# Performance work log

Measured on AMD Instinct MI355X. Metric: run time of the kernel, lower is better.

The kernel has to match this reference:

```python
import jax, jax.numpy as jnp
import numpy as np

D_MODEL = 1024
NUM_HEADS = 16
DEPTH = D_MODEL // NUM_HEADS


def setup_inputs() -> dict:
    key = jax.random.key(0)
    ks = jax.random.split(key, 12)
    B, S = 4, 2048
    scale = 1.0 / np.sqrt(D_MODEL)
    inp = {
        "query": jax.random.normal(ks[0], (B, S, D_MODEL), dtype=jnp.float32),
        "key": jax.random.normal(ks[1], (B, S, D_MODEL), dtype=jnp.float32),
        "value": jax.random.normal(ks[2], (B, S, D_MODEL), dtype=jnp.float32),
        "mask": jnp.zeros((B, 1, 1, S), dtype=jnp.float32),  # 1.0 = masked position
        "Wq": jax.random.normal(ks[3], (D_MODEL, D_MODEL), dtype=jnp.float32) * scale,
        "bq": jnp.zeros((D_MODEL,), dtype=jnp.float32),
        "Wk": jax.random.normal(ks[4], (D_MODEL, D_MODEL), dtype=jnp.float32) * scale,
        "bk": jnp.zeros((D_MODEL,), dtype=jnp.float32),
        "Wv": jax.random.normal(ks[5], (D_MODEL, D_MODEL), dtype=jnp.float32) * scale,
        "bv": jnp.zeros((D_MODEL,), dtype=jnp.float32),
        "Wo": jax.random.normal(ks[6], (D_MODEL, D_MODEL), dtype=jnp.float32) * scale,
        "bo": jnp.zeros((D_MODEL,), dtype=jnp.float32),
    }
    return inp


def _split_heads(x):
    # [B, S, D] -> [B, H, S, depth]
    B, S, _ = x.shape
    return x.reshape(B, S, NUM_HEADS, DEPTH).transpose(0, 2, 1, 3)


def reference(query, key, value, mask, Wq, bq, Wk, bk, Wv, bv, Wo, bo):
    B, Sq, _ = query.shape
    q = _split_heads(query @ Wq + bq)   # [B, H, Sq, d]
    k = _split_heads(key @ Wk + bk)     # [B, H, Sk, d]
    v = _split_heads(value @ Wv + bv)   # [B, H, Sk, d]
    logits = jnp.einsum('bhqd,bhkd->bhqk', q, k) / jnp.sqrt(jnp.float32(DEPTH))
    logits = logits + mask * (-1e9)
    attn = jax.nn.softmax(logits, axis=-1)
    ctx = jnp.einsum('bhqk,bhkd->bhqd', attn, v)        # [B, H, Sq, d]
    ctx = ctx.transpose(0, 2, 1, 3).reshape(B, Sq, D_MODEL)
    return ctx @ Wo + bo
```

## Files before the change

kernel.cpp:

```cpp
#include <hip/hip_runtime.h>
#include <math.h>

#define BB 4
#define SS 2048
#define DDM 1024
#define HH 16
#define MM (BB * SS)

typedef _Float16 f16;
typedef f16 half8 __attribute__((ext_vector_type(8)));
typedef f16 f16x4 __attribute__((ext_vector_type(4)));
typedef float f32x4 __attribute__((ext_vector_type(4)));

#define GLOAD16(g, l)                                                  \
  __builtin_amdgcn_global_load_lds(                                    \
      (const __attribute__((address_space(1))) void*)(g),              \
      (__attribute__((address_space(3))) void*)(l), 16, 0, 0)

__global__ void cvt_f16_k(const float* __restrict__ in, f16* __restrict__ out,
                          int n4) {
  int i = blockIdx.x * blockDim.x + threadIdx.x;
  const int stride = gridDim.x * blockDim.x;
  for (; i < n4; i += stride) {
    const float4 v = reinterpret_cast<const float4*>(in)[i];
    f16x4 o;
    o.x = (f16)v.x; o.y = (f16)v.y; o.z = (f16)v.z; o.w = (f16)v.w;
    reinterpret_cast<f16x4*>(out)[i] = o;
  }
}

__global__ void wtr_k(const float* __restrict__ W, f16* __restrict__ Wt) {
  __shared__ float t[32][33];
  const int bx = blockIdx.x * 32, by = blockIdx.y * 32;
  const int tx = threadIdx.x, ty = threadIdx.y;
#pragma unroll
  for (int i = 0; i < 4; ++i)
    t[ty + i * 8][tx] = W[(size_t)(by + ty + i * 8) * DDM + bx + tx];
  __syncthreads();
#pragma unroll
  for (int i = 0; i < 4; ++i)
    Wt[(size_t)(bx + ty + i * 8) * DDM + by + tx] = (f16)t[tx][ty + i * 8];
}

__global__ __launch_bounds__(256, 2) void gemm_f16_k(
    const f16* __restrict__ A, const f16* __restrict__ Bt,
    const float* __restrict__ bias, void* __restrict__ out, int mode) {
  __shared__ f16 Al[2][128 * 64];
  __shared__ f16 Bl[2][128 * 64];
  const int tid = threadIdx.x;
  const int l = tid & 63, w = tid >> 6;
  const int lr = l & 15, lg = l >> 4;
  const int wr = w >> 1, wc = w & 1;
  const int bm = blockIdx.x << 7, bn = blockIdx.y << 7;

  f32x4 acc[4][4];
#pragma unroll
  for (int m = 0; m < 4; ++m)
#pragma unroll
    for (int n = 0; n < 4; ++n) acc[m][n] = (f32x4){0.f, 0.f, 0.f, 0.f};

  const int srow = tid >> 3;
  const int scol = (tid & 7) ^ (srow & 7);
  const f16* Ap = A + (size_t)(bm + srow) * DDM + scol * 8;
  const f16* Bp = Bt + (size_t)(bn + srow) * DDM + scol * 8;
  const int kx = lr & 7;

#define G_STAGE(buf, kk)                                                     \
  do {                                                                       \
    _Pragma("unroll") for (int it = 0; it < 4; ++it) {                       \
      GLOAD16(Ap + (size_t)(it * 32) * DDM + (kk),                           \
              &Al[buf][(it * 256 + w * 64) * 8]);                            \
      GLOAD16(Bp + (size_t)(it * 32) * DDM + (kk),                           \
              &Bl[buf][(it * 256 + w * 64) * 8]);                            \
    }                                                                        \
  } while (0)

  G_STAGE(0, 0);
  __syncthreads();

  for (int kk = 0; kk < DDM; kk += 64) {
    const int cur = (kk >> 6) & 1;
    if (kk + 64 < DDM) G_STAGE(cur ^ 1, kk + 64);
#pragma unroll
    for (int kh = 0; kh < 2; ++kh) {
      half8 af[4], bf[4];
#pragma unroll
      for (int m = 0; m < 4; ++m) {
        const int row = wr * 64 + m * 16 + lr;
        af[m] = *reinterpret_cast<const half8*>(
            &Al[cur][row * 64 + (((kh * 4 + lg) ^ kx) * 8)]);
      }
#pragma unroll
      for (int n = 0; n < 4; ++n) {
        const int row = wc * 64 + n * 16 + lr;
        bf[n] = *reinterpret_cast<const half8*>(
            &Bl[cur][row * 64 + (((kh * 4 + lg) ^ kx) * 8)]);
      }
#pragma unroll
      for (int m = 0; m < 4; ++m)
#pragma unroll
        for (int n = 0; n < 4; ++n)
          acc[m][n] = __builtin_amdgcn_mfma_f32_16x16x32_f16(af[m], bf[n],
                                                             acc[m][n], 0, 0, 0);
    }
    __syncthreads();
  }
#undef G_STAGE

#pragma unroll
  for (int n = 0; n < 4; ++n) {
    const int gn = bn + wc * 64 + n * 16 + lr;
    const float bv = bias[gn];
#pragma unroll
    for (int m = 0; m < 4; ++m) {
      const int gm0 = bm + wr * 64 + m * 16 + lg * 4;
      if (mode == 2) {
        const int b = gm0 >> 11, s = gm0 & (SS - 1);
        const int h = gn >> 6, d = gn & 63;
        f16x4 o;
#pragma unroll
        for (int r = 0; r < 4; ++r) o[r] = (f16)(acc[m][n][r] + bv);
        *reinterpret_cast<f16x4*>(
            reinterpret_cast<f16*>(out) +
            (((size_t)(b * HH + h) * 64 + d) * SS + s)) = o;
      } else {
#pragma unroll
        for (int r = 0; r < 4; ++r) {
          const int gm = gm0 + r;
          const float v = acc[m][n][r] + bv;
          if (mode == 0) {
            reinterpret_cast<float*>(out)[(size_t)gm * DDM + gn] = v;
          } else {
            const int b = gm >> 11, s = gm & (SS - 1);
            const int h = gn >> 6, d = gn & 63;
            reinterpret_cast<f16*>(
                out)[(((size_t)(b * HH + h) * SS + s) << 6) + d] = (f16)v;
          }
        }
      }
    }
  }
}

__global__ __launch_bounds__(256, 2) void attn_f16_k(
    const f16* __restrict__ Q, const f16* __restrict__ K,
    const f16* __restrict__ Vt, const float* __restrict__ mask,
    f16* __restrict__ ctx) {
  __shared__ f16 Kl[2][64 * 64];
  __shared__ f16 Vl[2][64 * 64];
  __shared__ f16 Pl[4 * 16 * 66];
  __shared__ float Ml[SS];

  const int tid = threadIdx.x;
  const int l = tid & 63, w = tid >> 6;
  const int lr = l & 15, lg = l >> 4;
  const int qt = blockIdx.x;
  const int bh = blockIdx.y;
  const int b = bh >> 4, h = bh & 15;

  for (int i = tid; i < SS; i += 256) Ml[i] = mask[(size_t)b * SS + i] * -1e9f;

  const size_t qrow = (size_t)bh * SS + qt * 64 + w * 16 + lr;
  half8 qf0 = *reinterpret_cast<const half8*>(Q + qrow * 64 + lg * 8);
  half8 qf1 = *reinterpret_cast<const half8*>(Q + qrow * 64 + 32 + lg * 8);

  float m_s[4], l_s[4];
  f32x4 oa[4];
#pragma unroll
  for (int r = 0; r < 4; ++r) { m_s[r] = -1e30f; l_s[r] = 0.f; }
#pragma unroll
  for (int n = 0; n < 4; ++n) oa[n] = (f32x4){0.f, 0.f, 0.f, 0.f};

  const f16* Kg = K + (size_t)bh * SS * 64;
  const f16* Vg = Vt + (size_t)bh * 64 * SS;

  const int srow = tid >> 3;
  const int scol = (tid & 7) ^ (srow & 7);
  const int kx = lr & 7;
  f16* Pw = Pl + w * (16 * 66);

#define A_STAGE(buf, kt)                                                     \
  do {                                                                       \
    const f16* Kt_ = Kg + (size_t)(kt) * 64 * 64;                            \
    GLOAD16(Kt_ + srow * 64 + scol * 8, &Kl[buf][(w * 64) * 8]);             \
    GLOAD16(Kt_ + (32 + srow) * 64 + scol * 8,                               \
            &Kl[buf][(256 + w * 64) * 8]);                                   \
    const f16* Vr_ = Vg + (size_t)(kt) * 64 + scol * 8;                      \
    GLOAD16(Vr_ + (size_t)srow * SS, &Vl[buf][(w * 64) * 8]);                \
    GLOAD16(Vr_ + (size_t)(32 + srow) * SS, &Vl[buf][(256 + w * 64) * 8]);   \
  } while (0)

  A_STAGE(0, 0);
  __syncthreads();

  for (int kt = 0; kt < 32; ++kt) {
    const int cur = kt & 1;
    if (kt + 1 < 32) A_STAGE(cur ^ 1, kt + 1);

    f32x4 sv[4];
#pragma unroll
    for (int n = 0; n < 4; ++n) {
      f32x4 s = (f32x4){0.f, 0.f, 0.f, 0.f};
      const int krow = (n * 16 + lr) * 64;
      half8 kf0 = *reinterpret_cast<const half8*>(
          &Kl[cur][krow + ((lg ^ kx) * 8)]);
      half8 kf1 = *reinterpret_cast<const half8*>(
          &Kl[cur][krow + (((4 + lg) ^ kx) * 8)]);
      s = __builtin_amdgcn_mfma_f32_16x16x32_f16(qf0, kf0, s, 0, 0, 0);
      s = __builtin_amdgcn_mfma_f32_16x16x32_f16(qf1, kf1, s, 0, 0, 0);
      const float mk = Ml[kt * 64 + n * 16 + lr];
#pragma unroll
      for (int r = 0; r < 4; ++r) sv[n][r] = s[r] * 0.125f + mk;
    }

#pragma unroll
    for (int r = 0; r < 4; ++r) {
      float mx = fmaxf(fmaxf(sv[0][r], sv[1][r]), fmaxf(sv[2][r], sv[3][r]));
      mx = fmaxf(mx, __shfl_xor(mx, 1));
      mx = fmaxf(mx, __shfl_xor(mx, 2));
      mx = fmaxf(mx, __shfl_xor(mx, 4));
      mx = fmaxf(mx, __shfl_xor(mx, 8));
      const float mn = fmaxf(m_s[r], mx);
      const float corr = __expf(m_s[r] - mn);
      float sum = 0.f;
#pragma unroll
      for (int n = 0; n < 4; ++n) {
        const float p = __expf(sv[n][r] - mn);
        sv[n][r] = p;
        sum += p;
      }
      sum += __shfl_xor(sum, 1);
      sum += __shfl_xor(sum, 2);
      sum += __shfl_xor(sum, 4);
      sum += __shfl_xor(sum, 8);
      l_s[r] = l_s[r] * corr + sum;
      m_s[r] = mn;
#pragma unroll
      for (int n = 0; n < 4; ++n) oa[n][r] *= corr;
    }

#pragma unroll
    for (int n = 0; n < 4; ++n)
#pragma unroll
      for (int r = 0; r < 4; ++r)
        Pw[(lg * 4 + r) * 66 + n * 16 + lr] = (f16)sv[n][r];

    half8 pa0 = *reinterpret_cast<const half8*>(Pw + lr * 66 + lg * 8);
    half8 pa1 = *reinterpret_cast<const half8*>(Pw + lr * 66 + 32 + lg * 8);
#pragma unroll
    for (int n = 0; n < 4; ++n) {
      const int vrow = (n * 16 + lr) * 64;
      half8 vf0 = *reinterpret_cast<const half8*>(
          &Vl[cur][vrow + ((lg ^ kx) * 8)]);
      half8 vf1 = *reinterpret_cast<const half8*>(
          &Vl[cur][vrow + (((4 + lg) ^ kx) * 8)]);
      oa[n] = __builtin_amdgcn_mfma_f32_16x16x32_f16(pa0, vf0, oa[n], 0, 0, 0);
      oa[n] = __builtin_amdgcn_mfma_f32_16x16x32_f16(pa1, vf1, oa[n], 0, 0, 0);
    }
    __syncthreads();
  }
#undef A_STAGE

#pragma unroll
  for (int r = 0; r < 4; ++r) {
    const float inv = 1.0f / l_s[r];
    const int s_g = qt * 64 + w * 16 + lg * 4 + r;
#pragma unroll
    for (int n = 0; n < 4; ++n)
      ctx[((size_t)b * SS + s_g) * DDM + h * 64 + n * 16 + lr] =
          (f16)(oa[n][r] * inv);
  }
}

extern "C" void kernel_launch(void* const* d_in, const int* in_sizes, int n_in,
                              void* d_out, int out_size, void* d_ws,
                              size_t ws_size, hipStream_t stream) {
  const float* query = (const float*)d_in[0];
  const float* key   = (const float*)d_in[1];
  const float* value = (const float*)d_in[2];
  const float* mask  = (const float*)d_in[3];
  const float* Wq = (const float*)d_in[4];
  const float* bq = (const float*)d_in[5];
  const float* Wk = (const float*)d_in[6];
  const float* bk = (const float*)d_in[7];
  const float* Wv = (const float*)d_in[8];
  const float* bv = (const float*)d_in[9];
  const float* Wo = (const float*)d_in[10];
  const float* bo = (const float*)d_in[11];
  float* out = (float*)d_out;

  const size_t E = (size_t)MM * DDM;
  f16* ws = (f16*)d_ws;
  f16* Qh = ws;
  f16* Kh = Qh + E;
  f16* Vh = Kh + E;
  f16* Wt0 = Vh + E;
  f16* Wt1 = Wt0 + (size_t)DDM * DDM;
  f16* Wt2 = Wt1 + (size_t)DDM * DDM;
  f16* Wt3 = Wt2 + (size_t)DDM * DDM;
  f16* Qp = Wt3 + (size_t)DDM * DDM;
  f16* Kp = Qp + E;
  f16* Vp = Kp + E;
  f16* Ch = Vp + E;

  const int n4 = (int)(E / 4);
  cvt_f16_k<<<2048, 256, 0, stream>>>(query, Qh, n4);
  cvt_f16_k<<<2048, 256, 0, stream>>>(key, Kh, n4);
  cvt_f16_k<<<2048, 256, 0, stream>>>(value, Vh, n4);
  dim3 tb(32, 8), tg(32, 32);
  wtr_k<<<tg, tb, 0, stream>>>(Wq, Wt0);
  wtr_k<<<tg, tb, 0, stream>>>(Wk, Wt1);
  wtr_k<<<tg, tb, 0, stream>>>(Wv, Wt2);
  wtr_k<<<tg, tb, 0, stream>>>(Wo, Wt3);

  dim3 gg(MM / 128, DDM / 128);
  gemm_f16_k<<<gg, 256, 0, stream>>>(Qh, Wt0, bq, Qp, 1);
  gemm_f16_k<<<gg, 256, 0, stream>>>(Kh, Wt1, bk, Kp, 1);
  gemm_f16_k<<<gg, 256, 0, stream>>>(Vh, Wt2, bv, Vp, 2);
  attn_f16_k<<<dim3(SS / 64, BB * HH), 256, 0, stream>>>(Qp, Kp, Vp, mask, Ch);
  gemm_f16_k<<<gg, 256, 0, stream>>>(Ch, Wt3, bo, out, 0);
}
```

Before: 525.8 us.

## Double attention query tile, lazy rescale, single-buffer GEMM, merge prep kernels

The attention kernel now handles 128 query rows per block (32 per wave), so each K/V tile loaded into LDS is reused across twice as many rows. It pre-scales Q by 1/8, uses exp2 with log2e folded in, and rescales the running output only when a row max increases. The mask is read directly from global memory instead of being staged in LDS. The GEMM drops LDS double buffering to raise occupancy (launch bounds 4), at the cost of exposing load latency behind a barrier every k-step, and the convert and transpose launches are merged into single kernels.

```diff
diff --git a/kernel.cpp b/kernel.cpp
--- a/kernel.cpp
+++ b/kernel.cpp
@@ -17,20 +17,28 @@
       (const __attribute__((address_space(1))) void*)(g),              \
       (__attribute__((address_space(3))) void*)(l), 16, 0, 0)
 
-__global__ void cvt_f16_k(const float* __restrict__ in, f16* __restrict__ out,
-                          int n4) {
+__global__ void cvt3_k(const float* __restrict__ q, const float* __restrict__ k,
+                       const float* __restrict__ v, f16* __restrict__ oq,
+                       f16* __restrict__ ok, f16* __restrict__ ov, int n4) {
+  const float* in = (blockIdx.y == 0) ? q : (blockIdx.y == 1) ? k : v;
+  f16* out = (blockIdx.y == 0) ? oq : (blockIdx.y == 1) ? ok : ov;
   int i = blockIdx.x * blockDim.x + threadIdx.x;
   const int stride = gridDim.x * blockDim.x;
   for (; i < n4; i += stride) {
-    const float4 v = reinterpret_cast<const float4*>(in)[i];
+    const float4 t = reinterpret_cast<const float4*>(in)[i];
     f16x4 o;
-    o.x = (f16)v.x; o.y = (f16)v.y; o.z = (f16)v.z; o.w = (f16)v.w;
+    o.x = (f16)t.x; o.y = (f16)t.y; o.z = (f16)t.z; o.w = (f16)t.w;
     reinterpret_cast<f16x4*>(out)[i] = o;
   }
 }
 
-__global__ void wtr_k(const float* __restrict__ W, f16* __restrict__ Wt) {
+__global__ void wtr4_k(const float* __restrict__ Wq, const float* __restrict__ Wk,
+                       const float* __restrict__ Wv, const float* __restrict__ Wo,
+                       f16* __restrict__ Wt_all) {
   __shared__ float t[32][33];
+  const int z = blockIdx.z;
+  const float* W = (z == 0) ? Wq : (z == 1) ? Wk : (z == 2) ? Wv : Wo;
+  f16* Wt = Wt_all + (size_t)z * DDM * DDM;
   const int bx = blockIdx.x * 32, by = blockIdx.y * 32;
   const int tx = threadIdx.x, ty = threadIdx.y;
 #pragma unroll
@@ -42,11 +50,11 @@
     Wt[(size_t)(bx + ty + i * 8) * DDM + by + tx] = (f16)t[tx][ty + i * 8];
 }
 
-__global__ __launch_bounds__(256, 2) void gemm_f16_k(
+__global__ __launch_bounds__(256, 4) void gemm_f16_k(
     const f16* __restrict__ A, const f16* __restrict__ Bt,
     const float* __restrict__ bias, void* __restrict__ out, int mode) {
-  __shared__ f16 Al[2][128 * 64];
-  __shared__ f16 Bl[2][128 * 64];
+  __shared__ f16 Al[128 * 64];
+  __shared__ f16 Bl[128 * 64];
   const int tid = threadIdx.x;
   const int l = tid & 63, w = tid >> 6;
   const int lr = l & 15, lg = l >> 4;
@@ -65,22 +73,13 @@
   const f16* Bp = Bt + (size_t)(bn + srow) * DDM + scol * 8;
   const int kx = lr & 7;
 
-#define G_STAGE(buf, kk)                                                     \
-  do {                                                                       \
-    _Pragma("unroll") for (int it = 0; it < 4; ++it) {                       \
-      GLOAD16(Ap + (size_t)(it * 32) * DDM + (kk),                           \
-              &Al[buf][(it * 256 + w * 64) * 8]);                            \
-      GLOAD16(Bp + (size_t)(it * 32) * DDM + (kk),                           \
-              &Bl[buf][(it * 256 + w * 64) * 8]);                            \
-    }                                                                        \
-  } while (0)
-
-  G_STAGE(0, 0);
-  __syncthreads();
-
   for (int kk = 0; kk < DDM; kk += 64) {
-    const int cur = (kk >> 6) & 1;
-    if (kk + 64 < DDM) G_STAGE(cur ^ 1, kk + 64);
+#pragma unroll
+    for (int it = 0; it < 4; ++it) {
+      GLOAD16(Ap + (size_t)(it * 32) * DDM + kk, Al + (it * 256 + w * 64) * 8);
+      GLOAD16(Bp + (size_t)(it * 32) * DDM + kk, Bl + (it * 256 + w * 64) * 8);
+    }
+    __syncthreads();
 #pragma unroll
     for (int kh = 0; kh < 2; ++kh) {
       half8 af[4], bf[4];
@@ -88,13 +87,13 @@
       for (int m = 0; m < 4; ++m) {
         const int row = wr * 64 + m * 16 + lr;
         af[m] = *reinterpret_cast<const half8*>(
-            &Al[cur][row * 64 + (((kh * 4 + lg) ^ kx) * 8)]);
+            Al + row * 64 + (((kh * 4 + lg) ^ kx) * 8));
       }
 #pragma unroll
       for (int n = 0; n < 4; ++n) {
         const int row = wc * 64 + n * 16 + lr;
         bf[n] = *reinterpret_cast<const half8*>(
-            &Bl[cur][row * 64 + (((kh * 4 + lg) ^ kx) * 8)]);
+            Bl + row * 64 + (((kh * 4 + lg) ^ kx) * 8));
       }
 #pragma unroll
       for (int m = 0; m < 4; ++m)
@@ -105,7 +104,6 @@
     }
     __syncthreads();
   }
-#undef G_STAGE
 
 #pragma unroll
   for (int n = 0; n < 4; ++n) {
@@ -142,14 +140,13 @@
   }
 }
 
-__global__ __launch_bounds__(256, 2) void attn_f16_k(
+__global__ __launch_bounds__(256, 3) void attn_f16_k(
     const f16* __restrict__ Q, const f16* __restrict__ K,
     const f16* __restrict__ Vt, const float* __restrict__ mask,
     f16* __restrict__ ctx) {
   __shared__ f16 Kl[2][64 * 64];
   __shared__ f16 Vl[2][64 * 64];
-  __shared__ f16 Pl[4 * 16 * 66];
-  __shared__ float Ml[SS];
+  __shared__ f16 Pl[4][32 * 66];
 
   const int tid = threadIdx.x;
   const int l = tid & 63, w = tid >> 6;
@@ -158,26 +155,42 @@
   const int bh = blockIdx.y;
   const int b = bh >> 4, h = bh & 15;
 
-  for (int i = tid; i < SS; i += 256) Ml[i] = mask[(size_t)b * SS + i] * -1e9f;
-
-  const size_t qrow = (size_t)bh * SS + qt * 64 + w * 16 + lr;
-  half8 qf0 = *reinterpret_cast<const half8*>(Q + qrow * 64 + lg * 8);
-  half8 qf1 = *reinterpret_cast<const half8*>(Q + qrow * 64 + 32 + lg * 8);
-
-  float m_s[4], l_s[4];
-  f32x4 oa[4];
-#pragma unroll
-  for (int r = 0; r < 4; ++r) { m_s[r] = -1e30f; l_s[r] = 0.f; }
-#pragma unroll
-  for (int n = 0; n < 4; ++n) oa[n] = (f32x4){0.f, 0.f, 0.f, 0.f};
+  const float LOG2E = 1.44269504f;
+  const float NEGML2 = -1e9f * 1.44269504f;
+
+  half8 qf[2][2];
+  const size_t qbase = (size_t)bh * SS + qt * 128 + w * 32;
+#pragma unroll
+  for (int m = 0; m < 2; ++m) {
+    const size_t qrow = qbase + m * 16 + lr;
+#pragma unroll
+    for (int hh = 0; hh < 2; ++hh) {
+      half8 v = *reinterpret_cast<const half8*>(Q + qrow * 64 + hh * 32 + lg * 8);
+#pragma unroll
+      for (int j = 0; j < 8; ++j) v[j] = v[j] * (f16)0.125f;
+      qf[m][hh] = v;
+    }
+  }
+
+  float m_s[2][4], l_s[2][4];
+  f32x4 oa[2][4];
+#pragma unroll
+  for (int m = 0; m < 2; ++m)
+#pragma unroll
+    for (int r = 0; r < 4; ++r) { m_s[m][r] = -1e30f; l_s[m][r] = 0.f; }
+#pragma unroll
+  for (int m = 0; m < 2; ++m)
+#pragma unroll
+    for (int n = 0; n < 4; ++n) oa[m][n] = (f32x4){0.f, 0.f, 0.f, 0.f};
 
   const f16* Kg = K + (size_t)bh * SS * 64;
   const f16* Vg = Vt + (size_t)bh * 64 * SS;
+  const float* mrow = mask + (size_t)b * SS;
 
   const int srow = tid >> 3;
   const int scol = (tid & 7) ^ (srow & 7);
   const int kx = lr & 7;
-  f16* Pw = Pl + w * (16 * 66);
+  f16* Pw = Pl[w];
 
 #define A_STAGE(buf, kt)                                                     \
   do {                                                                       \
@@ -197,56 +210,82 @@
     const int cur = kt & 1;
     if (kt + 1 < 32) A_STAGE(cur ^ 1, kt + 1);
 
-    f32x4 sv[4];
+    float mk[4];
+#pragma unroll
+    for (int n = 0; n < 4; ++n) mk[n] = mrow[kt * 64 + n * 16 + lr] * NEGML2;
+
+    f32x4 sv[2][4];
 #pragma unroll
     for (int n = 0; n < 4; ++n) {
-      f32x4 s = (f32x4){0.f, 0.f, 0.f, 0.f};
       const int krow = (n * 16 + lr) * 64;
       half8 kf0 = *reinterpret_cast<const half8*>(
           &Kl[cur][krow + ((lg ^ kx) * 8)]);
       half8 kf1 = *reinterpret_cast<const half8*>(
           &Kl[cur][krow + (((4 + lg) ^ kx) * 8)]);
-      s = __builtin_amdgcn_mfma_f32_16x16x32_f16(qf0, kf0, s, 0, 0, 0);
-      s = __builtin_amdgcn_mfma_f32_16x16x32_f16(qf1, kf1, s, 0, 0, 0);
-      const float mk = Ml[kt * 64 + n * 16 + lr];
-#pragma unroll
-      for (int r = 0; r < 4; ++r) sv[n][r] = s[r] * 0.125f + mk;
-    }
-
-#pragma unroll
-    for (int r = 0; r < 4; ++r) {
-      float mx = fmaxf(fmaxf(sv[0][r], sv[1][r]), fmaxf(sv[2][r], sv[3][r]));
-      mx = fmaxf(mx, __shfl_xor(mx, 1));
-      mx = fmaxf(mx, __shfl_xor(mx, 2));
-      mx = fmaxf(mx, __shfl_xor(mx, 4));
-      mx = fmaxf(mx, __shfl_xor(mx, 8));
-      const float mn = fmaxf(m_s[r], mx);
-      const float corr = __expf(m_s[r] - mn);
-      float sum = 0.f;
-#pragma unroll
-      for (int n = 0; n < 4; ++n) {
-        const float p = __expf(sv[n][r] - mn);
-        sv[n][r] = p;
-        sum += p;
-      }
-      sum += __shfl_xor(sum, 1);
-      sum += __shfl_xor(sum, 2);
-      sum += __shfl_xor(sum, 4);
-      sum += __shfl_xor(sum, 8);
-      l_s[r] = l_s[r] * corr + sum;
-      m_s[r] = mn;
-#pragma unroll
-      for (int n = 0; n < 4; ++n) oa[n][r] *= corr;
-    }
-
-#pragma unroll
-    for (int n = 0; n < 4; ++n)
-#pragma unroll
-      for (int r = 0; r < 4; ++r)
-        Pw[(lg * 4 + r) * 66 + n * 16 + lr] = (f16)sv[n][r];
-
-    half8 pa0 = *reinterpret_cast<const half8*>(Pw + lr * 66 + lg * 8);
-    half8 pa1 = *reinterpret_cast<const half8*>(Pw + lr * 66 + 32 + lg * 8);
+#pragma unroll
+      for (int m = 0; m < 2; ++m) {
+        f32x4 s = (f32x4){0.f, 0.f, 0.f, 0.f};
+        s = __builtin_amdgcn_mfma_f32_16x16x32_f16(qf[m][0], kf0, s, 0, 0, 0);
+        s = __builtin_amdgcn_mfma_f32_16x16x32_f16(qf[m][1], kf1, s, 0, 0, 0);
+#pragma unroll
+        for (int r = 0; r < 4; ++r) sv[m][n][r] = fmaf(s[r], LOG2E, mk[n]);
+      }
+    }
+
+    float mx[2][4];
+    bool need = false;
+#pragma unroll
+    for (int m = 0; m < 2; ++m)
+#pragma unroll
+      for (int r = 0; r < 4; ++r) {
+        float t0 = fmaxf(fmaxf(sv[m][0][r], sv[m][1][r]),
+                         fmaxf(sv[m][2][r], sv[m][3][r]));
+        t0 = fmaxf(t0, __shfl_xor(t0, 1));
+        t0 = fmaxf(t0, __shfl_xor(t0, 2));
+        t0 = fmaxf(t0, __shfl_xor(t0, 4));
+        t0 = fmaxf(t0, __shfl_xor(t0, 8));
+        mx[m][r] = t0;
+        need |= (t0 > m_s[m][r]);
+      }
+    if (__any(need)) {
+#pragma unroll
+      for (int m = 0; m < 2; ++m)
+#pragma unroll
+        for (int r = 0; r < 4; ++r) {
+          const float mn = fmaxf(m_s[m][r], mx[m][r]);
+          const float corr = exp2f(m_s[m][r] - mn);
+          l_s[m][r] *= corr;
+          m_s[m][r] = mn;
+#pragma unroll
+          for (int n = 0; n < 4; ++n) oa[m][n][r] *= corr;
+        }
+    }
+
+#pragma unroll
+    for (int m = 0; m < 2; ++m)
+#pragma unroll
+      for (int r = 0; r < 4; ++r) {
+        float sum = 0.f;
+#pragma unroll
+        for (int n = 0; n < 4; ++n) {
+          const float p = exp2f(sv[m][n][r] - m_s[m][r]);
+          sum += p;
+          Pw[(m * 16 + lg * 4 + r) * 66 + n * 16 + lr] = (f16)p;
+        }
+        sum += __shfl_xor(sum, 1);
+        sum += __shfl_xor(sum, 2);
+        sum += __shfl_xor(sum, 4);
+        sum += __shfl_xor(sum, 8);
+        l_s[m][r] += sum;
+      }
+
+    half8 pa[2][2];
+#pragma unroll
+    for (int m = 0; m < 2; ++m)
+#pragma unroll
+      for (int hh = 0; hh < 2; ++hh)
+        pa[m][hh] = *reinterpret_cast<const half8*>(
+            Pw + (m * 16 + lr) * 66 + hh * 32 + lg * 8);
 #pragma unroll
     for (int n = 0; n < 4; ++n) {
       const int vrow = (n * 16 + lr) * 64;
@@ -254,22 +293,29 @@
           &Vl[cur][vrow + ((lg ^ kx) * 8)]);
       half8 vf1 = *reinterpret_cast<const half8*>(
           &Vl[cur][vrow + (((4 + lg) ^ kx) * 8)]);
-      oa[n] = __builtin_amdgcn_mfma_f32_16x16x32_f16(pa0, vf0, oa[n], 0, 0, 0);
-      oa[n] = __builtin_amdgcn_mfma_f32_16x16x32_f16(pa1, vf1, oa[n], 0, 0, 0);
+#pragma unroll
+      for (int m = 0; m < 2; ++m) {
+        oa[m][n] = __builtin_amdgcn_mfma_f32_16x16x32_f16(pa[m][0], vf0,
+                                                          oa[m][n], 0, 0, 0);
+        oa[m][n] = __builtin_amdgcn_mfma_f32_16x16x32_f16(pa[m][1], vf1,
+                                                          oa[m][n], 0, 0, 0);
+      }
     }
     __syncthreads();
   }
 #undef A_STAGE
 
 #pragma unroll
-  for (int r = 0; r < 4; ++r) {
-    const float inv = 1.0f / l_s[r];
-    const int s_g = qt * 64 + w * 16 + lg * 4 + r;
-#pragma unroll
-    for (int n = 0; n < 4; ++n)
-      ctx[((size_t)b * SS + s_g) * DDM + h * 64 + n * 16 + lr] =
-          (f16)(oa[n][r] * inv);
-  }
+  for (int m = 0; m < 2; ++m)
+#pragma unroll
+    for (int r = 0; r < 4; ++r) {
+      const float inv = 1.0f / l_s[m][r];
+      const int s_g = qt * 128 + w * 32 + m * 16 + lg * 4 + r;
+#pragma unroll
+      for (int n = 0; n < 4; ++n)
+        ctx[((size_t)b * SS + s_g) * DDM + h * 64 + n * 16 + lr] =
+            (f16)(oa[m][n][r] * inv);
+    }
 }
 
 extern "C" void kernel_launch(void* const* d_in, const int* in_sizes, int n_in,
@@ -295,28 +341,20 @@
   f16* Kh = Qh + E;
   f16* Vh = Kh + E;
   f16* Wt0 = Vh + E;
-  f16* Wt1 = Wt0 + (size_t)DDM * DDM;
-  f16* Wt2 = Wt1 + (size_t)DDM * DDM;
-  f16* Wt3 = Wt2 + (size_t)DDM * DDM;
-  f16* Qp = Wt3 + (size_t)DDM * DDM;
+  f16* Wt3 = Wt0 + (size_t)3 * DDM * DDM;
+  f16* Qp = Wt0 + (size_t)4 * DDM * DDM;
   f16* Kp = Qp + E;
   f16* Vp = Kp + E;
   f16* Ch = Vp + E;
 
   const int n4 = (int)(E / 4);
-  cvt_f16_k<<<2048, 256, 0, stream>>>(query, Qh, n4);
-  cvt_f16_k<<<2048, 256, 0, stream>>>(key, Kh, n4);
-  cvt_f16_k<<<2048, 256, 0, stream>>>(value, Vh, n4);
-  dim3 tb(32, 8), tg(32, 32);
-  wtr_k<<<tg, tb, 0, stream>>>(Wq, Wt0);
-  wtr_k<<<tg, tb, 0, stream>>>(Wk, Wt1);
-  wtr_k<<<tg, tb, 0, stream>>>(Wv, Wt2);
-  wtr_k<<<tg, tb, 0, stream>>>(Wo, Wt3);
+  cvt3_k<<<dim3(1024, 3), 256, 0, stream>>>(query, key, value, Qh, Kh, Vh, n4);
+  wtr4_k<<<dim3(32, 32, 4), dim3(32, 8), 0, stream>>>(Wq, Wk, Wv, Wo, Wt0);
 
   dim3 gg(MM / 128, DDM / 128);
   gemm_f16_k<<<gg, 256, 0, stream>>>(Qh, Wt0, bq, Qp, 1);
-  gemm_f16_k<<<gg, 256, 0, stream>>>(Kh, Wt1, bk, Kp, 1);
-  gemm_f16_k<<<gg, 256, 0, stream>>>(Vh, Wt2, bv, Vp, 2);
-  attn_f16_k<<<dim3(SS / 64, BB * HH), 256, 0, stream>>>(Qp, Kp, Vp, mask, Ch);
+  gemm_f16_k<<<gg, 256, 0, stream>>>(Kh, Wt0 + (size_t)DDM * DDM, bk, Kp, 1);
+  gemm_f16_k<<<gg, 256, 0, stream>>>(Vh, Wt0 + (size_t)2 * DDM * DDM, bv, Vp, 2);
+  attn_f16_k<<<dim3(SS / 128, BB * HH), 256, 0, stream>>>(Qp, Kp, Vp, mask, Ch);
   gemm_f16_k<<<gg, 256, 0, stream>>>(Ch, Wt3, bo, out, 0);
 }
```

After: 529.2 us. Within noise of the previous version (+0.7%).
